# Performance work log

Measured on AMD Instinct MI355X. Metric: run time of the kernel, lower is better.

The kernel has to match this reference:

```python
import jax, jax.numpy as jnp
import numpy as np

N = 8192        # batch_size (number of nodes)
E = 262144      # number of edges
VD = 256        # vertex_dim
ED = 256        # edge_dim
HD = 512        # hid_dim
DAMPING = 0.45
EPS = 1e-5      # BatchNorm1d default eps


def setup_inputs() -> dict:
    key = jax.random.key(0)
    ks = jax.random.split(key, 8)
    def lin_w(k, out_d, in_d):
        # kaiming-uniform-ish scale, fp32
        lim = 1.0 / np.sqrt(in_d)
        return jax.random.uniform(k, (out_d, in_d), jnp.float32, -lim, lim)
    return {
        "x": jax.random.normal(ks[0], (N, VD), jnp.float32),
        "edge_weight": jax.random.normal(ks[1], (E, ED), jnp.float32),
        "edge_index": jax.random.randint(ks[2], (2, E), 0, N),
        "W0": lin_w(ks[3], HD, VD), "b0": jnp.zeros((HD,), jnp.float32),
        "Ww0": lin_w(ks[4], HD, ED), "bw0": jnp.zeros((HD,), jnp.float32),
        "W1": lin_w(ks[5], VD, HD), "b1": jnp.zeros((VD,), jnp.float32),
        "Ww1": lin_w(ks[6], ED, HD), "bw1": jnp.zeros((ED,), jnp.float32),
        "gamma": jnp.ones((HD,), jnp.float32),
        "beta": jnp.zeros((HD,), jnp.float32),
    }


def reference(x, edge_weight, edge_index, W0, b0, Ww0, bw0, W1, b1, Ww1, bw1, gamma, beta):
    out = x @ W0.T + b0                       # [N, HD]
    w = edge_weight @ Ww0.T + bw0             # [E, HD]
    src = edge_index[0]                       # [E]
    # The per-node python loop in the original is an exact segment reduction:
    # out[i] += damping * sum of w over edges with src==i (pre-update w),
    # then w[e] += damping * scalar_sum(out_new[src[e]])  (t.sum over hid dim).
    out = out + DAMPING * jax.ops.segment_sum(w, src, num_segments=N)
    node_scalar = jnp.sum(out, axis=1)        # [N] scalar per node
    w = w + DAMPING * node_scalar[src][:, None]
    # cauchy selector: cosine similarity minus identity, row-softmax mix
    nrm = jnp.sqrt(jnp.sum(out * out, axis=1, keepdims=True))   # [N,1]
    sim = (out @ out.T) / (nrm @ nrm.T) - jnp.eye(N, dtype=out.dtype)
    out = jax.nn.softmax(sim, axis=1) @ out   # [N, HD]
    # BatchNorm1d in training mode (batch stats, biased variance)
    mean = jnp.mean(w, axis=0)
    var = jnp.mean((w - mean) ** 2, axis=0)
    w = (w - mean) * jax.lax.rsqrt(var + EPS) * gamma + beta
    return out @ W1.T + b1, w @ Ww1.T + bw1
```

## Files before the change

kernel.cpp:

```cpp
#include <hip/hip_runtime.h>

typedef unsigned short u16;
typedef __attribute__((ext_vector_type(8))) short bh8;
typedef __attribute__((ext_vector_type(4))) short bh4;
typedef __attribute__((ext_vector_type(4))) float f4v;

#define NN 8192
#define EE 262144
#define VDIM 256
#define EDIM 256
#define HDIM 512
#define DAMP 0.45f

__device__ __forceinline__ float b2f(u16 u){ unsigned int x = ((unsigned int)u)<<16; return __builtin_bit_cast(float, x); }
__device__ __forceinline__ u16 f2b(float f){ unsigned int x = __builtin_bit_cast(unsigned int, f); x = (x + 0x7fffu + ((x>>16)&1u)) >> 16; return (u16)x; }

__device__ __forceinline__ void gload16(const void* g, void* l){
  __builtin_amdgcn_global_load_lds((const __attribute__((address_space(1))) void*)g,
                                   (__attribute__((address_space(3))) void*)l, 16, 0, 0);
}

__global__ __launch_bounds__(256) void k_hist(const int* __restrict__ src, int* __restrict__ deg){
  int e = blockIdx.x*256 + threadIdx.x;
  if (e < EE) atomicAdd(&deg[src[e]], 1);
}

__global__ __launch_bounds__(1024) void k_scan(const int* __restrict__ deg, int* __restrict__ ofs, int* __restrict__ cur){
  __shared__ int lds[1024];
  int t = threadIdx.x;
  int v[8], pre[8]; int s = 0;
  #pragma unroll
  for (int j=0;j<8;++j){ v[j] = deg[t*8+j]; }
  #pragma unroll
  for (int j=0;j<8;++j){ pre[j] = s; s += v[j]; }
  lds[t] = s; __syncthreads();
  int run = s;
  for (int off=1; off<1024; off<<=1){
    int x = (t>=off) ? lds[t-off] : 0;
    __syncthreads();
    lds[t] += x;
    __syncthreads();
  }
  int excl = lds[t] - run;
  #pragma unroll
  for (int j=0;j<8;++j){ int o = excl + pre[j]; ofs[t*8+j] = o; cur[t*8+j] = o; }
  if (t == 1023) ofs[NN] = excl + run;
}

__global__ __launch_bounds__(256) void k_permute(const int* __restrict__ src, int* __restrict__ cur,
                                                 int* __restrict__ pos, int* __restrict__ elist){
  int e = blockIdx.x*256 + threadIdx.x;
  if (e < EE){ int p = atomicAdd(&cur[src[e]], 1); pos[e] = p; elist[p] = e; }
}

__global__ __launch_bounds__(256) void k_cvtW(const float* __restrict__ in, u16* __restrict__ out, int n8){
  int i = blockIdx.x*256 + threadIdx.x;
  if (i < n8){
    const f4v* p = (const f4v*)(in + (size_t)i*8);
    f4v f0 = p[0], f1 = p[1];
    bh8 v;
    #pragma unroll
    for (int j=0;j<4;++j){ v[j]=(short)f2b(f0[j]); v[j+4]=(short)f2b(f1[j]); }
    ((bh8*)out)[i] = v;
  }
}

template<int A_BF16, int B_BF16, int EPI>
__global__ __launch_bounds__(256)
void k_gemm(const void* __restrict__ Aptr, const void* __restrict__ Bptr,
            int M, int N, int K, const float* __restrict__ bias,
            void* __restrict__ Cptr,
            const float* __restrict__ invnA, float* __restrict__ lsum)
{
  __shared__ u16 As[128*32];
  __shared__ u16 Bs[128*32];
  __shared__ float lrow[128];
  const int t = threadIdx.x;
  const int m0 = blockIdx.y*128, n0 = blockIdx.x*128;
  const int wid = t>>6, lane = t&63, l15 = lane&15, grp = lane>>4;
  const int wm = (wid>>1)*64, wn = (wid&1)*64;
  const int srow = t>>1, shalf = t&1;
  const int rlane = lane>>2, clane = lane&3;

  if (EPI == 3 && t < 128) lrow[t] = 0.f;

  f4v acc[4][4];
  #pragma unroll
  for (int i=0;i<4;++i)
    #pragma unroll
    for (int j=0;j<4;++j) acc[i][j] = (f4v)0.0f;

  for (int kt=0; kt<K; kt+=32){
    __syncthreads();
    if (A_BF16){
      const u16* g0 = (const u16*)Aptr + (size_t)(m0 + wid*32 + rlane)*K + kt + clane*8;
      gload16(g0,                 &As[wid*1024]);
      gload16(g0 + (size_t)16*K,  &As[wid*1024 + 512]);
    } else {
      u16* dst = &As[srow*32 + shalf*16];
      const float* ap = (const float*)Aptr + (size_t)(m0+srow)*K + kt + shalf*16;
      const f4v* ap4 = (const f4v*)ap;
      f4v f0 = ap4[0], f1 = ap4[1], f2 = ap4[2], f3 = ap4[3];
      bh8 v0, v1;
      #pragma unroll
      for (int j=0;j<4;++j){ v0[j]=(short)f2b(f0[j]); v0[j+4]=(short)f2b(f1[j]); v1[j]=(short)f2b(f2[j]); v1[j+4]=(short)f2b(f3[j]); }
      ((bh8*)dst)[0] = v0; ((bh8*)dst)[1] = v1;
    }
    if (B_BF16){
      const u16* g0 = (const u16*)Bptr + (size_t)(n0 + wid*32 + rlane)*K + kt + clane*8;
      gload16(g0,                 &Bs[wid*1024]);
      gload16(g0 + (size_t)16*K,  &Bs[wid*1024 + 512]);
    } else {
      u16* dst = &Bs[srow*32 + shalf*16];
      const float* bp = (const float*)Bptr + (size_t)(n0+srow)*K + kt + shalf*16;
      const f4v* bp4 = (const f4v*)bp;
      f4v f0 = bp4[0], f1 = bp4[1], f2 = bp4[2], f3 = bp4[3];
      bh8 v0, v1;
      #pragma unroll
      for (int j=0;j<4;++j){ v0[j]=(short)f2b(f0[j]); v0[j+4]=(short)f2b(f1[j]); v1[j]=(short)f2b(f2[j]); v1[j+4]=(short)f2b(f3[j]); }
      ((bh8*)dst)[0] = v0; ((bh8*)dst)[1] = v1;
    }
    __syncthreads();
    bh8 af[4], bfv[4];
    #pragma unroll
    for (int f=0; f<4; ++f) af[f]  = *(const bh8*)&As[(wm + f*16 + l15)*32 + grp*8];
    #pragma unroll
    for (int f=0; f<4; ++f) bfv[f] = *(const bh8*)&Bs[(wn + f*16 + l15)*32 + grp*8];
    #pragma unroll
    for (int fi=0; fi<4; ++fi)
      #pragma unroll
      for (int fj=0; fj<4; ++fj)
        acc[fi][fj] = __builtin_amdgcn_mfma_f32_16x16x32_bf16(af[fi], bfv[fj], acc[fi][fj], 0, 0, 0);
  }

  if (EPI == 3){
    float ic[4];
    #pragma unroll
    for (int fj=0; fj<4; ++fj) ic[fj] = invnA[n0 + wn + fj*16 + l15];
    #pragma unroll
    for (int fi=0; fi<4; ++fi){
      #pragma unroll
      for (int r=0;r<4;++r){
        int rowg = m0 + wm + fi*16 + grp*4 + r;
        float iq = invnA[rowg];
        float rs = 0.f;
        #pragma unroll
        for (int fj=0; fj<4; ++fj){
          int c = n0 + wn + fj*16 + l15;
          float s = acc[fi][fj][r]*iq*ic[fj];
          float p = (rowg == c) ? 1.0f : __expf(s);
          ((u16*)Cptr)[(size_t)rowg*N + c] = f2b(p);
          rs += p;
        }
        rs += __shfl_xor(rs,1); rs += __shfl_xor(rs,2); rs += __shfl_xor(rs,4); rs += __shfl_xor(rs,8);
        if (l15 == 0) atomicAdd(&lrow[wm + fi*16 + grp*4 + r], rs);
      }
    }
    __syncthreads();
    if (t < 128) lsum[(size_t)blockIdx.x*NN + m0 + t] = lrow[t];
    return;
  }

  float ilv[4][4];
  if (EPI == 4){
    #pragma unroll
    for (int fi=0; fi<4; ++fi)
      #pragma unroll
      for (int r=0;r<4;++r)
        ilv[fi][r] = 1.0f / lsum[m0 + wm + fi*16 + grp*4 + r];
  }
  #pragma unroll
  for (int fj=0; fj<4; ++fj){
    int c = n0 + wn + fj*16 + l15;
    float bv = (EPI == 0 && bias) ? bias[c] : 0.f;
    #pragma unroll
    for (int fi=0; fi<4; ++fi){
      #pragma unroll
      for (int r=0;r<4;++r){
        size_t rowg = (size_t)(m0 + wm + fi*16 + grp*4 + r);
        float v = acc[fi][fj][r];
        if (EPI == 0)      ((float*)Cptr)[rowg*N + c] = v + bv;
        else               ((u16*)Cptr)[rowg*N + c]  = f2b(v * ilv[fi][r]);
      }
    }
  }
}

__global__ __launch_bounds__(256)
void k_lred(const float* __restrict__ lpart, float* __restrict__ lsum){
  int i = blockIdx.x*256 + threadIdx.x;
  float s = 0.f;
  #pragma unroll 8
  for (int b = 0; b < 64; ++b) s += lpart[(size_t)b*NN + i];
  lsum[i] = s;
}

template<int A_BF16, int BN, int EPI>
__global__ __launch_bounds__(512, 4)
void k_gemmw3(const void* __restrict__ Aptr, const u16* __restrict__ Bptr,
              int K, const float* __restrict__ bias, void* __restrict__ Cptr,
              const int* __restrict__ mapArr, const int* __restrict__ srcIdx,
              const float* __restrict__ nsArr, const float* __restrict__ rowterm,
              const float* __restrict__ constterm)
{
  constexpr int CG = BN/64;
  constexpr int MF = (CG==8)?4:2;
  __shared__ u16 As[64*32];
  __shared__ u16 Bs[BN*32];
  const int t = threadIdx.x;
  const int tile = ((int)blockIdx.x & 7)*((int)gridDim.x>>3) + ((int)blockIdx.x>>3);
  const int m0 = tile*64;
  const int wid = t>>6, lane = t&63, l15 = lane&15, grp = lane>>4;
  const int wn = (wid & (CG-1))*64;
  const int wm = (wid / CG)*32;

  f4v acc[MF][4];
  #pragma unroll
  for (int i=0;i<MF;++i)
    #pragma unroll
    for (int j=0;j<4;++j) acc[i][j] = (f4v)0.0f;

  if (A_BF16){
    if (wid < 4){
      const u16* g0 = (const u16*)Aptr + (size_t)(m0 + wid*16 + (lane>>2))*K + (lane&3)*8;
      gload16(g0, &As[wid*512]);
    }
  } else {
    const float* ap = (const float*)Aptr + (size_t)(m0 + (t>>3))*K + (t&7)*4;
    f4v f0 = *(const f4v*)ap;
    bh4 v;
    #pragma unroll
    for (int j=0;j<4;++j) v[j]=(short)f2b(f0[j]);
    *(bh4*)&As[(t>>3)*32 + (t&7)*4] = v;
  }
  #pragma unroll
  for (int j=0;j<BN/128;++j){
    const u16* g0 = Bptr + (size_t)(j*128 + wid*16 + (lane>>2))*K + (lane&3)*8;
    gload16(g0, &Bs[wid*512 + j*4096]);
  }
  __syncthreads();

  for (int kt=0; kt<K; kt+=32){
    const bool more = (kt+32 < K);
    f4v pf; bh8 pb;
    if (more){
      if (A_BF16){
        if (t < 256)
          pb = *(const bh8*)((const u16*)Aptr + (size_t)(m0 + (t>>2))*K + kt+32 + (t&3)*8);
      } else {
        pf = *(const f4v*)((const float*)Aptr + (size_t)(m0 + (t>>3))*K + kt+32 + (t&7)*4);
      }
    }
    bh8 af[MF], bfv[4];
    #pragma unroll
    for (int f=0; f<MF; ++f) af[f]  = *(const bh8*)&As[(wm + f*16 + l15)*32 + grp*8];
    #pragma unroll
    for (int f=0; f<4; ++f)  bfv[f] = *(const bh8*)&Bs[(wn + f*16 + l15)*32 + grp*8];
    #pragma unroll
    for (int fi=0; fi<MF; ++fi)
      #pragma unroll
      for (int fj=0; fj<4; ++fj)
        acc[fi][fj] = __builtin_amdgcn_mfma_f32_16x16x32_bf16(af[fi], bfv[fj], acc[fi][fj], 0, 0, 0);
    __syncthreads();
    if (more){
      if (A_BF16){
        if (t < 256) *(bh8*)&As[(t>>2)*32 + (t&3)*8] = pb;
      } else {
        bh4 v;
        #pragma unroll
        for (int j=0;j<4;++j) v[j]=(short)f2b(pf[j]);
        *(bh4*)&As[(t>>3)*32 + (t&7)*4] = v;
      }
      #pragma unroll
      for (int j=0;j<BN/128;++j){
        const u16* g0 = Bptr + (size_t)(j*128 + wid*16 + (lane>>2))*K + kt+32 + (lane&3)*8;
        gload16(g0, &Bs[wid*512 + j*4096]);
      }
    }
    __syncthreads();
  }

  #pragma unroll
  for (int fi=0; fi<MF; ++fi){
    #pragma unroll
    for (int r=0;r<4;++r){
      int slot = m0 + wm + fi*16 + grp*4 + r;
      int mp = mapArr[slot];
      float cv = (EPI == 2) ? DAMP * nsArr[srcIdx[mp]] : 0.f;
      #pragma unroll
      for (int fj=0; fj<4; ++fj){
        int c = wn + fj*16 + l15;
        if (EPI == 5) ((u16*)Cptr)[(size_t)mp*BN + c]  = f2b(acc[fi][fj][r] + bias[c]);
        else          ((float*)Cptr)[(size_t)mp*BN + c] = acc[fi][fj][r] + cv*rowterm[c] + constterm[c];
      }
    }
  }
}

__global__ __launch_bounds__(512, 8)
void k_segsumB(const u16* __restrict__ w0, const int* __restrict__ ofs,
               float* __restrict__ S, float* __restrict__ sqpart)
{
  __shared__ u16 lds[16*512];
  const int t = threadIdx.x, w = t>>6, lane = t&63;
  const int base = blockIdx.x*128;

  int lo = 0, hi = NN-1;
  while (lo < hi){ int mid = (lo+hi+1)>>1; if (ofs[mid] <= base) lo = mid; else hi = mid-1; }
  int ni = lo;
  int nend = ofs[ni+1];

  float acc = 0.f, sqv = 0.f;
  bool first = true;

  for (int chunk = 0; chunk < 8; ++chunk){
    __syncthreads();
    {
      const u16* r0 = w0 + (size_t)(base + chunk*16 + w)*512 + lane*8;
      gload16(r0,                  &lds[w*512]);
      gload16(r0 + (size_t)8*512,  &lds[(w+8)*512]);
    }
    __syncthreads();
    #pragma unroll
    for (int r = 0; r < 16; ++r){
      int row = base + chunk*16 + r;
      float v = b2f(lds[r*512 + t]);
      acc += v; sqv += v*v;
      if (row + 1 == nend){
        if (first){ atomicAdd(&S[(size_t)ni*512 + t], acc); first = false; }
        else        S[(size_t)ni*512 + t] = acc;
        acc = 0.f; ++ni;
        while (ni < NN-1 && ofs[ni+1] == row+1) ++ni;
        nend = ofs[ni+1];
      }
    }
  }
  if (base + 128 < nend) atomicAdd(&S[(size_t)ni*512 + t], acc);
  sqpart[(size_t)blockIdx.x*512 + t] = sqv;
}

__global__ __launch_bounds__(512)
void k_sqred(const float* __restrict__ sqpart, float* __restrict__ colsumsq){
  int t = threadIdx.x;
  float s = 0.f;
  for (int b = 0; b < 32; ++b)
    s += sqpart[(size_t)(blockIdx.x*32 + b)*512 + t];
  atomicAdd(&colsumsq[t], s);
}

__global__ __launch_bounds__(256)
void k_nodefin2(const float* __restrict__ S, const float* __restrict__ out0,
                float* __restrict__ nsA, float* __restrict__ invn, u16* __restrict__ ob)
{
  const int t = threadIdx.x, wid = t>>6, lane = t&63;
  const int node = blockIdx.x*4 + wid;
  const f4v* s4 = (const f4v*)(S + (size_t)node*512 + lane*8);
  f4v sA = s4[0], sB = s4[1];
  const f4v* o4 = (const f4v*)(out0 + (size_t)node*512 + lane*8);
  f4v qA = o4[0], qB = o4[1];
  float o[8];
  #pragma unroll
  for (int j=0;j<4;++j){ o[j] = qA[j] + DAMP*sA[j]; o[j+4] = qB[j] + DAMP*sB[j]; }
  float nsp = 0.f, qp = 0.f;
  #pragma unroll
  for (int j=0;j<8;++j){ nsp += o[j]; qp += o[j]*o[j]; }
  #pragma unroll
  for (int m=1; m<64; m<<=1){ nsp += __shfl_xor(nsp, m); qp += __shfl_xor(qp, m); }
  if (lane == 0){ nsA[node] = nsp; invn[node] = rsqrtf(qp); }
  bh8 ub;
  #pragma unroll
  for (int j=0;j<8;++j) ub[j] = (short)f2b(o[j]);
  *(bh8*)(ob + (size_t)node*512 + lane*8) = ub;
}

__global__ __launch_bounds__(512)
void k_colred(const float* __restrict__ S, const float* __restrict__ nsA,
              const int* __restrict__ ofs,
              float* __restrict__ colsum0, float* __restrict__ cross,
              float* __restrict__ sumc, float* __restrict__ sumc2)
{
  __shared__ float red1[128], red2[128];
  const int t = threadIdx.x;
  const int n0 = blockIdx.x*128;
  float cs = 0.f, cr = 0.f;
  for (int i = 0; i < 128; ++i){
    int node = n0 + i;
    float s = S[(size_t)node*512 + t];
    cs += s; cr += nsA[node]*s;
  }
  atomicAdd(&colsum0[t], cs);
  atomicAdd(&cross[t],   DAMP*cr);
  if (t < 128){
    int node = n0 + t;
    float nsv = nsA[node];
    float degf = (float)(ofs[node+1] - ofs[node]);
    red1[t] = degf*nsv;
    red2[t] = degf*nsv*nsv;
  }
  __syncthreads();
  if (t == 0){
    float s1 = 0.f, s2 = 0.f;
    #pragma unroll 8
    for (int i = 0; i < 128; ++i){ s1 += red1[i]; s2 += red2[i]; }
    atomicAdd(sumc,  DAMP*s1);
    atomicAdd(sumc2, DAMP*DAMP*s2);
  }
}

__global__ __launch_bounds__(256)
void k_transpose(const u16* __restrict__ in, u16* __restrict__ out){
  __shared__ u16 tile[64][65];
  int r0 = blockIdx.x*64, c0 = blockIdx.y*64;
  int t = threadIdx.x;
  int rr = t>>2, cc = (t&3)*16;
  const u16* ip = in + (size_t)(r0+rr)*512 + c0 + cc;
  #pragma unroll
  for (int j=0;j<16;++j) tile[rr][cc+j] = ip[j];
  __syncthreads();
  int cr = t>>2, rb = (t&3)*16;
  u16* op = out + (size_t)(c0+cr)*8192 + r0 + rb;
  #pragma unroll
  for (int j=0;j<16;++j) op[j] = tile[rb+j][cr];
}

__global__ __launch_bounds__(512)
void k_bnfinal(const float* __restrict__ colsum0, const float* __restrict__ colsumsq,
               const float* __restrict__ cross, const float* __restrict__ sumc,
               const float* __restrict__ sumc2, const float* __restrict__ gamma,
               const float* __restrict__ beta, float* __restrict__ alphaA, float* __restrict__ bbA)
{
  int j = threadIdx.x;
  const float invE = 1.0f / (float)EE;
  float mean = (colsum0[j] + sumc[0]) * invE;
  float ex2  = (colsumsq[j] + 2.f*cross[j] + sumc2[0]) * invE;
  float var  = ex2 - mean*mean;
  float is   = rsqrtf(var + 1e-5f);
  float a    = gamma[j]*is;
  alphaA[j]  = a;
  bbA[j]     = beta[j] - mean*a;
}

__global__ __launch_bounds__(512)
void k_wprime(const float* __restrict__ Ww1, const float* __restrict__ alphaA,
              const float* __restrict__ bbA, const float* __restrict__ bw1,
              u16* __restrict__ Ww1pb, float* __restrict__ rowterm, float* __restrict__ constt)
{
  __shared__ float red[512];
  int k = blockIdx.x, j = threadIdx.x;
  float wv = Ww1[(size_t)k*512 + j];
  float a  = alphaA[j];
  Ww1pb[(size_t)k*512 + j] = f2b(wv*a);
  red[j] = wv*a; __syncthreads();
  for (int off=256; off>0; off>>=1){ if (j<off) red[j] += red[j+off]; __syncthreads(); }
  if (j == 0) rowterm[k] = red[0];
  __syncthreads();
  red[j] = wv*bbA[j]; __syncthreads();
  for (int off=256; off>0; off>>=1){ if (j<off) red[j] += red[j+off]; __syncthreads(); }
  if (j == 0) constt[k] = red[0] + bw1[k];
}

extern "C" void kernel_launch(void* const* d_in, const int* in_sizes, int n_in,
                              void* d_out, int out_size, void* d_ws, size_t ws_size,
                              hipStream_t stream)
{
  const float* x    = (const float*)d_in[0];
  const float* ew   = (const float*)d_in[1];
  const int*   ei   = (const int*)  d_in[2];
  const float* W0   = (const float*)d_in[3];
  const float* b0   = (const float*)d_in[4];
  const float* Ww0  = (const float*)d_in[5];
  const float* bw0  = (const float*)d_in[6];
  const float* W1   = (const float*)d_in[7];
  const float* b1   = (const float*)d_in[8];
  const float* Ww1  = (const float*)d_in[9];
  const float* bw1  = (const float*)d_in[10];
  const float* gamma= (const float*)d_in[11];
  const float* beta = (const float*)d_in[12];
  const int* src = ei;

  char* ws = (char*)d_ws;
  u16*   w0    = (u16*)  (ws + 0ULL);
  float* out0  = (float*)(ws + 268435456ULL);
  u16*   ob    = (u16*)  (ws + 285212672ULL);
  u16*   obT   = (u16*)  (ws + 293601280ULL);
  u16*   onew  = (u16*)  (ws + 301989888ULL);
  float* nsA   = (float*)(ws + 310378496ULL);
  float* invn  = (float*)(ws + 310411264ULL);
  int*   deg   = (int*)  (ws + 310444032ULL);
  int*   ofs   = (int*)  (ws + 310476800ULL);
  int*   cur   = (int*)  (ws + 310509824ULL);
  int*   elist = (int*)  (ws + 310542592ULL);
  float* stats = (float*)(ws + 311591168ULL);
  float* cross    = stats;
  float* colsum0  = stats + 512;
  float* colsumsq = stats + 1024;
  float* sumc     = stats + 1536;
  float* sumc2    = stats + 1537;
  float* lsum   = (float*)(ws + 311607552ULL);
  u16*   Ww1pb  = (u16*)  (ws + 311640320ULL);
  float* rowterm= (float*)(ws + 312164608ULL);
  float* constt = (float*)(ws + 312165632ULL);
  float* alphaA = (float*)(ws + 312166656ULL);
  float* bbA    = (float*)(ws + 312168704ULL);
  u16*   Ww0b   = (u16*)  (ws + 312170752ULL);
  int*   pos   = (int*)onew;

  float* out1 = (float*)d_out;
  float* out2 = out1 + (size_t)NN*VDIM;
  u16*   Pbuf = (u16*)out2;
  float* lpart  = (float*)((char*)out2 + 167772160ULL);
  float* sqpart = (float*)((char*)out2 + 247463936ULL);
  float* S      = (float*)((char*)out2 + 251658240ULL);

  hipMemsetAsync(deg, 0, NN*sizeof(int), stream);
  hipMemsetAsync(stats, 0, 16384, stream);
  hipMemsetAsync(S, 0, (size_t)NN*512*sizeof(float), stream);

  k_hist   <<<EE/256, 256, 0, stream>>>(src, deg);
  k_scan   <<<1, 1024, 0, stream>>>(deg, ofs, cur);
  k_permute<<<EE/256, 256, 0, stream>>>(src, cur, pos, elist);
  k_cvtW   <<<64, 256, 0, stream>>>(Ww0, Ww0b, HDIM*EDIM/8);

  k_gemmw3<0,512,5><<<4096, 512, 0, stream>>>(ew, Ww0b, EDIM, bw0, w0,
                                              pos, nullptr, nullptr, nullptr, nullptr);
  k_gemm<0,0,0><<<dim3(4,64), 256, 0, stream>>>(x, W0, NN, HDIM, VDIM, b0, out0, nullptr, nullptr);

  k_segsumB<<<2048, 512, 0, stream>>>(w0, ofs, S, sqpart);
  k_sqred  <<<64, 512, 0, stream>>>(sqpart, colsumsq);
  k_nodefin2<<<NN/4, 256, 0, stream>>>(S, out0, nsA, invn, ob);
  k_colred <<<64, 512, 0, stream>>>(S, nsA, ofs, colsum0, cross, sumc, sumc2);

  k_transpose<<<dim3(128,8), 256, 0, stream>>>(ob, obT);
  k_bnfinal<<<1, 512, 0, stream>>>(colsum0, colsumsq, cross, sumc, sumc2, gamma, beta, alphaA, bbA);
  k_wprime<<<256, 512, 0, stream>>>(Ww1, alphaA, bbA, bw1, Ww1pb, rowterm, constt);

  k_gemm<1,1,3><<<dim3(64,64), 256, 0, stream>>>(ob, ob, NN, NN, HDIM, nullptr, Pbuf, invn, lpart);
  k_lred<<<NN/256, 256, 0, stream>>>(lpart, lsum);
  k_gemm<1,1,4><<<dim3(4,64), 256, 0, stream>>>(Pbuf, obT, NN, HDIM, NN, nullptr, onew, nullptr, lsum);

  k_gemmw3<1,256,2><<<4096, 512, 0, stream>>>(w0, Ww1pb, HDIM, nullptr, out2,
                                              elist, src, nsA, rowterm, constt);
  k_gemm<1,0,0><<<dim3(2,64), 256, 0, stream>>>(onew, W1, NN, VDIM, HDIM, b1, out1, nullptr, nullptr);
}
```

Baseline: 839.4 us.

## Fuse cosine-similarity softmax and PV product into a flash-attention style kernel

Replaces the three-step selector path with a fused kernel plus a small combine kernel. The old path materialised the full 8192x8192 bf16 probability matrix, reduced row sums in a separate pass and then ran a second GEMM over it. The new kernel computes QK^T tiles in LDS, exponentiates them, accumulates row sums and immediately multiplies by V. The key range is split in two halves and the partial outputs are combined in a finalize pass. This removes the large intermediate write and read, but each block re-streams all K/V tiles with no double-buffering and only one 136KB-LDS block fits per CU, so occupancy is low.

Measured after the change: 1.285 ms. 1.53x slower.

```diff
diff --git a/kernel.cpp b/kernel.cpp
--- a/kernel.cpp
+++ b/kernel.cpp
@@ -74,15 +74,12 @@
 {
   __shared__ u16 As[128*32];
   __shared__ u16 Bs[128*32];
-  __shared__ float lrow[128];
   const int t = threadIdx.x;
   const int m0 = blockIdx.y*128, n0 = blockIdx.x*128;
   const int wid = t>>6, lane = t&63, l15 = lane&15, grp = lane>>4;
   const int wm = (wid>>1)*64, wn = (wid&1)*64;
   const int srow = t>>1, shalf = t&1;
   const int rlane = lane>>2, clane = lane&3;
-
-  if (EPI == 3 && t < 128) lrow[t] = 0.f;
 
   f4v acc[4][4];
   #pragma unroll
@@ -133,66 +130,19 @@
         acc[fi][fj] = __builtin_amdgcn_mfma_f32_16x16x32_bf16(af[fi], bfv[fj], acc[fi][fj], 0, 0, 0);
   }
 
-  if (EPI == 3){
-    float ic[4];
-    #pragma unroll
-    for (int fj=0; fj<4; ++fj) ic[fj] = invnA[n0 + wn + fj*16 + l15];
-    #pragma unroll
-    for (int fi=0; fi<4; ++fi){
-      #pragma unroll
-      for (int r=0;r<4;++r){
-        int rowg = m0 + wm + fi*16 + grp*4 + r;
-        float iq = invnA[rowg];
-        float rs = 0.f;
-        #pragma unroll
-        for (int fj=0; fj<4; ++fj){
-          int c = n0 + wn + fj*16 + l15;
-          float s = acc[fi][fj][r]*iq*ic[fj];
-          float p = (rowg == c) ? 1.0f : __expf(s);
-          ((u16*)Cptr)[(size_t)rowg*N + c] = f2b(p);
-          rs += p;
-        }
-        rs += __shfl_xor(rs,1); rs += __shfl_xor(rs,2); rs += __shfl_xor(rs,4); rs += __shfl_xor(rs,8);
-        if (l15 == 0) atomicAdd(&lrow[wm + fi*16 + grp*4 + r], rs);
-      }
-    }
-    __syncthreads();
-    if (t < 128) lsum[(size_t)blockIdx.x*NN + m0 + t] = lrow[t];
-    return;
-  }
-
-  float ilv[4][4];
-  if (EPI == 4){
-    #pragma unroll
-    for (int fi=0; fi<4; ++fi)
-      #pragma unroll
-      for (int r=0;r<4;++r)
-        ilv[fi][r] = 1.0f / lsum[m0 + wm + fi*16 + grp*4 + r];
-  }
   #pragma unroll
   for (int fj=0; fj<4; ++fj){
     int c = n0 + wn + fj*16 + l15;
-    float bv = (EPI == 0 && bias) ? bias[c] : 0.f;
+    float bv = (bias) ? bias[c] : 0.f;
     #pragma unroll
     for (int fi=0; fi<4; ++fi){
       #pragma unroll
       for (int r=0;r<4;++r){
         size_t rowg = (size_t)(m0 + wm + fi*16 + grp*4 + r);
-        float v = acc[fi][fj][r];
-        if (EPI == 0)      ((float*)Cptr)[rowg*N + c] = v + bv;
-        else               ((u16*)Cptr)[rowg*N + c]  = f2b(v * ilv[fi][r]);
-      }
-    }
-  }
-}
-
-__global__ __launch_bounds__(256)
-void k_lred(const float* __restrict__ lpart, float* __restrict__ lsum){
-  int i = blockIdx.x*256 + threadIdx.x;
-  float s = 0.f;
-  #pragma unroll 8
-  for (int b = 0; b < 64; ++b) s += lpart[(size_t)b*NN + i];
-  lsum[i] = s;
+        ((float*)Cptr)[rowg*N + c] = acc[fi][fj][r] + bv;
+      }
+    }
+  }
 }
 
 template<int A_BF16, int BN, int EPI>
@@ -295,6 +245,131 @@
       }
     }
   }
+}
+
+__global__ __launch_bounds__(512)
+void k_fattn(const u16* __restrict__ ob, const u16* __restrict__ obT,
+             const float* __restrict__ invn,
+             float* __restrict__ Opart, float* __restrict__ lpart2)
+{
+  __shared__ u16 Ks[64*512];
+  __shared__ u16 Vs[512*64];
+  __shared__ u16 Pl[64*64];
+  __shared__ float lrow[64];
+  const int t = threadIdx.x, w = t>>6, lane = t&63, l15 = lane&15, grp = lane>>4;
+  const int qb = (int)blockIdx.x >> 1, z = (int)blockIdx.x & 1;
+  const int br = qb*64;
+  const int kvb = z*4096;
+  const int r0 = (w>>2)*32, c0 = (w&3)*16;
+
+  if (t < 64) lrow[t] = 0.f;
+
+  bh8 aq[2][16];
+  #pragma unroll
+  for (int fi=0; fi<2; ++fi){
+    const u16* qp = ob + (size_t)(br + r0 + fi*16 + l15)*512;
+    #pragma unroll
+    for (int ks=0; ks<16; ++ks) aq[fi][ks] = *(const bh8*)(qp + ks*32 + grp*8);
+  }
+  float invq[2][4];
+  #pragma unroll
+  for (int fi=0; fi<2; ++fi)
+    #pragma unroll
+    for (int r=0;r<4;++r) invq[fi][r] = invn[br + r0 + fi*16 + grp*4 + r];
+
+  f4v oacc[4][4];
+  #pragma unroll
+  for (int i=0;i<4;++i)
+    #pragma unroll
+    for (int j=0;j<4;++j) oacc[i][j] = (f4v)0.0f;
+
+  for (int it=0; it<64; ++it){
+    const int kv0 = kvb + it*64;
+    __syncthreads();
+    #pragma unroll
+    for (int j=0;j<8;++j){
+      int r = w + 8*j;
+      const u16* g = ob + (size_t)(kv0 + r)*512 + ((lane ^ w)<<3);
+      gload16(g, &Ks[r*512]);
+    }
+    #pragma unroll
+    for (int j=0;j<8;++j){
+      int d0 = w*64 + j*8;
+      const u16* g = obT + (size_t)(d0 + (lane>>3))*8192 + kv0 + (((lane&7) ^ (lane>>3))<<3);
+      gload16(g, &Vs[d0*64]);
+    }
+    __syncthreads();
+
+    const int kr = c0 + l15;
+    const int kmsk = (kr&7)<<3;
+    const float invk = invn[kv0 + kr];
+    #pragma unroll
+    for (int fi=0; fi<2; ++fi){
+      f4v sacc = (f4v)0.0f;
+      #pragma unroll
+      for (int ks=0; ks<16; ++ks){
+        bh8 bq = *(const bh8*)&Ks[kr*512 + ((ks*32 + grp*8) ^ kmsk)];
+        sacc = __builtin_amdgcn_mfma_f32_16x16x32_bf16(aq[fi][ks], bq, sacc, 0,0,0);
+      }
+      #pragma unroll
+      for (int r=0;r<4;++r){
+        int prow = r0 + fi*16 + grp*4 + r;
+        float s = sacc[r]*invq[fi][r]*invk;
+        float p = ((br + prow) == (kv0 + kr)) ? 1.0f : __expf(s);
+        Pl[prow*64 + (kr ^ ((prow&7)<<3))] = f2b(p);
+        float rs = p;
+        rs += __shfl_xor(rs,1); rs += __shfl_xor(rs,2); rs += __shfl_xor(rs,4); rs += __shfl_xor(rs,8);
+        if (l15 == 0) atomicAdd(&lrow[prow], rs);
+      }
+    }
+    __syncthreads();
+
+    #pragma unroll
+    for (int ks2=0; ks2<2; ++ks2){
+      bh8 pa[4];
+      #pragma unroll
+      for (int afi=0; afi<4; ++afi){
+        int prow = afi*16 + l15;
+        pa[afi] = *(const bh8*)&Pl[prow*64 + ((ks2*32 + grp*8) ^ ((prow&7)<<3))];
+      }
+      #pragma unroll
+      for (int cfj=0; cfj<4; ++cfj){
+        int vrow = w*64 + cfj*16 + l15;
+        bh8 bv = *(const bh8*)&Vs[vrow*64 + ((ks2*32 + grp*8) ^ ((vrow&7)<<3))];
+        #pragma unroll
+        for (int afi=0; afi<4; ++afi)
+          oacc[afi][cfj] = __builtin_amdgcn_mfma_f32_16x16x32_bf16(pa[afi], bv, oacc[afi][cfj], 0,0,0);
+      }
+    }
+  }
+  __syncthreads();
+  #pragma unroll
+  for (int afi=0; afi<4; ++afi){
+    #pragma unroll
+    for (int r=0;r<4;++r){
+      size_t ro = (size_t)z*NN*512 + (size_t)(br + afi*16 + grp*4 + r)*512;
+      #pragma unroll
+      for (int cfj=0; cfj<4; ++cfj)
+        Opart[ro + w*64 + cfj*16 + l15] = oacc[afi][cfj][r];
+    }
+  }
+  if (t < 64) lpart2[(size_t)z*NN + br + t] = lrow[t];
+}
+
+__global__ __launch_bounds__(256)
+void k_fin(const float* __restrict__ Opart, const float* __restrict__ lpart2,
+           u16* __restrict__ onew)
+{
+  int idx = blockIdx.x*256 + threadIdx.x;
+  int row = idx >> 7;
+  int c4 = (idx & 127) << 2;
+  float il = 1.0f / (lpart2[row] + lpart2[NN + row]);
+  f4v a = *(const f4v*)&Opart[(size_t)row*512 + c4];
+  f4v b = *(const f4v*)&Opart[(size_t)NN*512 + (size_t)row*512 + c4];
+  ushort4 o;
+  o.x = f2b((a[0]+b[0])*il); o.y = f2b((a[1]+b[1])*il);
+  o.z = f2b((a[2]+b[2])*il); o.w = f2b((a[3]+b[3])*il);
+  *(ushort4*)&onew[(size_t)row*512 + c4] = o;
 }
 
 __global__ __launch_bounds__(512, 8)
@@ -496,7 +571,6 @@
   float* colsumsq = stats + 1024;
   float* sumc     = stats + 1536;
   float* sumc2    = stats + 1537;
-  float* lsum   = (float*)(ws + 311607552ULL);
   u16*   Ww1pb  = (u16*)  (ws + 311640320ULL);
   float* rowterm= (float*)(ws + 312164608ULL);
   float* constt = (float*)(ws + 312165632ULL);
@@ -507,8 +581,8 @@
 
   float* out1 = (float*)d_out;
   float* out2 = out1 + (size_t)NN*VDIM;
-  u16*   Pbuf = (u16*)out2;
-  float* lpart  = (float*)((char*)out2 + 167772160ULL);
+  float* Opart  = (float*)out2;
+  float* lpart2 = (float*)((char*)out2 + 33554432ULL);
   float* sqpart = (float*)((char*)out2 + 247463936ULL);
   float* S      = (float*)((char*)out2 + 251658240ULL);
 
@@ -534,9 +608,8 @@
   k_bnfinal<<<1, 512, 0, stream>>>(colsum0, colsumsq, cross, sumc, sumc2, gamma, beta, alphaA, bbA);
   k_wprime<<<256, 512, 0, stream>>>(Ww1, alphaA, bbA, bw1, Ww1pb, rowterm, constt);
 
-  k_gemm<1,1,3><<<dim3(64,64), 256, 0, stream>>>(ob, ob, NN, NN, HDIM, nullptr, Pbuf, invn, lpart);
-  k_lred<<<NN/256, 256, 0, stream>>>(lpart, lsum);
-  k_gemm<1,1,4><<<dim3(4,64), 256, 0, stream>>>(Pbuf, obT, NN, HDIM, NN, nullptr, onew, nullptr, lsum);
+  k_fattn<<<256, 512, 0, stream>>>(ob, obT, invn, Opart, lpart2);
+  k_fin  <<<NN*512/1024, 256, 0, stream>>>(Opart, lpart2, onew);
 
   k_gemmw3<1,256,2><<<4096, 512, 0, stream>>>(w0, Ww1pb, HDIM, nullptr, out2,
                                               elist, src, nsA, rowterm, constt);
```
